# Kernel optimization log

Measured on AMD Instinct MI355X. Metric: run time of the kernel, lower is better.

The kernel has to match this reference:

```python
import jax, jax.numpy as jnp
import numpy as np

NUM_ATOMS = 100000
NUM_BONDS = 200000
MAX_NB = 6
ATOM_FDIM = 133
BOND_FDIM = 147
HIDDEN = 300
DEPTH = 4
NUM_MOLS = 8192


def setup_inputs() -> dict:
    key = jax.random.key(0)
    ks = jax.random.split(key, 10)
    f_atoms = jax.random.normal(ks[0], (NUM_ATOMS, ATOM_FDIM), dtype=jnp.float32)
    f_bonds = jax.random.normal(ks[1], (NUM_BONDS, BOND_FDIM), dtype=jnp.float32)
    a2b = jax.random.randint(ks[2], (NUM_ATOMS, MAX_NB), 0, NUM_BONDS, dtype=jnp.int32)
    b2a = jax.random.randint(ks[3], (NUM_BONDS,), 0, NUM_ATOMS, dtype=jnp.int32)
    b2revb = jax.random.randint(ks[4], (NUM_BONDS,), 0, NUM_BONDS, dtype=jnp.int32)
    mol_ids = jnp.sort(jax.random.randint(ks[5], (NUM_ATOMS,), 0, NUM_MOLS, dtype=jnp.int32))
    s = 1.0 / np.sqrt(HIDDEN)
    W_i = jax.random.uniform(ks[6], (BOND_FDIM, HIDDEN), jnp.float32, -s, s)
    W_h = jax.random.uniform(ks[7], (HIDDEN, HIDDEN), jnp.float32, -s, s)
    W_o = jax.random.uniform(ks[8], (ATOM_FDIM + HIDDEN, HIDDEN), jnp.float32, -s, s)
    b_o = jax.random.uniform(ks[9], (HIDDEN,), jnp.float32, -s, s)
    return {"f_atoms": f_atoms, "f_bonds": f_bonds, "W_i": W_i, "W_h": W_h,
            "W_o": W_o, "b_o": b_o, "a2b": a2b, "b2a": b2a, "b2revb": b2revb,
            "mol_ids": mol_ids}


def reference(f_atoms, f_bonds, W_i, W_h, W_o, b_o, a2b, b2a, b2revb, mol_ids):
    # initial bond messages: W_i then activation (bias=False)
    inp = f_bonds @ W_i                       # [B, H]
    message = jax.nn.relu(inp)
    for _ in range(DEPTH - 1):
        nei = message[a2b]                    # [A, MAX_NB, H] gather
        a_message = nei.sum(axis=1)           # [A, H]
        rev_message = message[b2revb]         # [B, H]
        message = a_message[b2a] - rev_message
        message = jax.nn.relu(inp + message @ W_h)
    # final atom readout
    a_message = message[a2b].sum(axis=1)      # [A, H]
    a_input = jnp.concatenate([f_atoms, a_message], axis=1)
    atom_hiddens = jax.nn.relu(a_input @ W_o + b_o)
    # per-molecule mean aggregation (== chemprop a_scope loop with 'mean')
    sums = jax.ops.segment_sum(atom_hiddens, mol_ids, num_segments=NUM_MOLS)
    counts = jax.ops.segment_sum(jnp.ones((NUM_ATOMS,), jnp.float32), mol_ids,
                                 num_segments=NUM_MOLS)
    return sums / jnp.maximum(counts, 1.0)[:, None]
```

## Files before the change

### kernel.cpp

```cpp
#include <hip/hip_runtime.h>


#define DEVFN static __device__ __forceinline__

typedef __attribute__((ext_vector_type(8))) __bf16 bf16x8;
typedef __attribute__((ext_vector_type(4))) float floatx4;

DEVFN unsigned short f2bf(float f) {
    unsigned int u = __float_as_uint(f);
    u += 0x7FFFu + ((u >> 16) & 1u);
    return (unsigned short)(u >> 16);
}
DEVFN float bf2f(unsigned int u) { return __uint_as_float(u << 16); }

DEVFN unsigned int bfsub2(unsigned int a, unsigned int m) {
    float lo = bf2f(a & 0xffffu) - bf2f(m & 0xffffu);
    float hi = bf2f(a >> 16) - bf2f(m >> 16);
    return (unsigned int)f2bf(lo) | ((unsigned int)f2bf(hi) << 16);
}
DEVFN uint4 bfsub8(uint4 a, uint4 m) {
    return make_uint4(bfsub2(a.x, m.x), bfsub2(a.y, m.y),
                      bfsub2(a.z, m.z), bfsub2(a.w, m.w));
}

__global__ __launch_bounds__(256) void dbg_fill(float* out, int n, float v) {
    int t = blockIdx.x * 256 + threadIdx.x;
    if (t < n) out[t] = v;
}

__global__ __launch_bounds__(256) void prep_wih(const float* __restrict__ Wi,
                                                const float* __restrict__ Wh,
                                                unsigned short* __restrict__ Wt) {
    int t = blockIdx.x * 256 + threadIdx.x;
    if (t >= 320 * 480) return;
    int n = t / 480, k = t - n * 480;
    float v = 0.f;
    if (n < 300) {
        if (k < 147) v = Wi[k * 300 + n];
        else if (k >= 160 && k < 460) v = Wh[(k - 160) * 300 + n];
    }
    Wt[t] = f2bf(v);
}

__global__ __launch_bounds__(256) void prep_wto(const float* __restrict__ Wo,
                                                unsigned short* __restrict__ Wt) {
    int t = blockIdx.x * 256 + threadIdx.x;
    if (t >= 320 * 448) return;
    int n = t / 448, k = t - n * 448;
    float v = 0.f;
    if (n < 300) {
        if (k < 300) v = Wo[(133 + k) * 300 + n];
        else if (k >= 304 && k < 437) v = Wo[(k - 304) * 300 + n];
    }
    Wt[t] = f2bf(v);
}

__global__ __launch_bounds__(256) void pad_bonds(const float* __restrict__ fb,
                                                 unsigned short* __restrict__ out) {
    int t = blockIdx.x * 256 + threadIdx.x;
    if (t >= 200000 * 20) return;
    int b = t / 20, c = t - b * 20;
    unsigned int o[4];
#pragma unroll
    for (int p = 0; p < 4; ++p) {
        int sc = c * 8 + p * 2;
        float v0 = (sc < 147) ? fb[(size_t)b * 147 + sc] : 0.f;
        float v1 = (sc + 1 < 147) ? fb[(size_t)b * 147 + sc + 1] : 0.f;
        o[p] = (unsigned int)f2bf(v0) | ((unsigned int)f2bf(v1) << 16);
    }
    *(uint4*)(out + (size_t)b * 160 + c * 8) = make_uint4(o[0], o[1], o[2], o[3]);
}

__global__ __launch_bounds__(256) void atoms_concat(const float* __restrict__ fa,
                                                    unsigned short* __restrict__ concat) {
    int t = blockIdx.x * 256 + threadIdx.x;
    if (t >= 100000 * 18) return;
    int a = t / 18, c = t - a * 18;
    unsigned int o[4];
#pragma unroll
    for (int p = 0; p < 4; ++p) {
        int sc = c * 8 + p * 2;
        float v0 = (sc < 133) ? fa[(size_t)a * 133 + sc] : 0.f;
        float v1 = (sc + 1 < 133) ? fa[(size_t)a * 133 + sc + 1] : 0.f;
        o[p] = (unsigned int)f2bf(v0) | ((unsigned int)f2bf(v1) << 16);
    }
    *(uint4*)(concat + (size_t)a * 448 + 304 + c * 8) = make_uint4(o[0], o[1], o[2], o[3]);
}

template <int CH>
__global__ __launch_bounds__(256) void gather_sum(const unsigned short* __restrict__ msg,
                                                  const int* __restrict__ a2b,
                                                  unsigned short* __restrict__ out,
                                                  int ostride, int nA) {
    int t = blockIdx.x * 256 + threadIdx.x;
    if (t >= nA * CH) return;
    int a = t / CH, c = t - a * CH;
    float s[8] = {0, 0, 0, 0, 0, 0, 0, 0};
#pragma unroll
    for (int j = 0; j < 6; ++j) {
        int b = a2b[a * 6 + j];
        uint4 v = *(const uint4*)(msg + (size_t)b * 320 + c * 8);
        s[0] += bf2f(v.x & 0xffffu); s[1] += bf2f(v.x >> 16);
        s[2] += bf2f(v.y & 0xffffu); s[3] += bf2f(v.y >> 16);
        s[4] += bf2f(v.z & 0xffffu); s[5] += bf2f(v.z >> 16);
        s[6] += bf2f(v.w & 0xffffu); s[7] += bf2f(v.w >> 16);
    }
    unsigned int o[4];
#pragma unroll
    for (int p = 0; p < 4; ++p)
        o[p] = (unsigned int)f2bf(s[2 * p]) | ((unsigned int)f2bf(s[2 * p + 1]) << 16);
    *(uint4*)(out + (size_t)a * ostride + c * 8) = make_uint4(o[0], o[1], o[2], o[3]);
}

template <int KT0, int KT1, int MODE, int BSTRIDE>
__global__ __launch_bounds__(256) void gemm_k(const unsigned short* __restrict__ A0,
                                              int a0s,
                                              const unsigned short* __restrict__ amsg,
                                              const unsigned short* __restrict__ msg,
                                              const int* __restrict__ b2a,
                                              const int* __restrict__ b2revb,
                                              const unsigned short* __restrict__ Wt,
                                              unsigned short* __restrict__ outp,
                                              float* __restrict__ hid,
                                              const float* __restrict__ bo, int M) {
    constexpr int KT = KT0 + KT1;
    __shared__ unsigned short As[2 * 5120];
    __shared__ unsigned short Bs[2 * 5120];

    const int tid = threadIdx.x;
    const int lane = tid & 63;
    const int wave = tid >> 6;
    const int wm = wave & 1, wn = wave >> 1;
    const int l16 = lane & 15, quad = lane >> 4;
    const int m0 = blockIdx.x * 128;
    const int n0 = blockIdx.y * 160;

    const int arow = tid >> 1, ahalf = tid & 1;
    const int gr = min(m0 + arow, M - 1);
    const unsigned short* a0p = A0 + (size_t)gr * a0s + ahalf * 16;
    const unsigned short* a1p = nullptr;
    const unsigned short* m1p = nullptr;
    if (KT1 > 0) {
        a1p = amsg + (size_t)b2a[gr] * 320 + ahalf * 16;
        m1p = msg + (size_t)b2revb[gr] * 320 + ahalf * 16;
    }
    const int u0 = tid, u1 = tid + 256, u2 = tid + 512;
    const unsigned short* bg0 = Wt + (size_t)(n0 + (u0 >> 2)) * BSTRIDE + ((u0 ^ (u0 >> 2)) & 3) * 8;
    const unsigned short* bg1 = Wt + (size_t)(n0 + (u1 >> 2)) * BSTRIDE + ((u1 ^ (u1 >> 2)) & 3) * 8;
    const unsigned short* bg2 = (tid < 128)
        ? Wt + (size_t)(n0 + (u2 >> 2)) * BSTRIDE + ((u2 ^ (u2 >> 2)) & 3) * 8 : Wt;

    int aoff[4], boff[5];
#pragma unroll
    for (int tm = 0; tm < 4; ++tm)
        aoff[tm] = (wm * 64 + tm * 16 + l16) * 40 + quad * 8;
#pragma unroll
    for (int tn = 0; tn < 5; ++tn) {
        int nl = wn * 80 + tn * 16 + l16;
        boff[tn] = nl * 32 + ((quad ^ nl) & 3) * 8;
    }

    floatx4 acc[4][5];
#pragma unroll
    for (int tm = 0; tm < 4; ++tm)
#pragma unroll
        for (int tn = 0; tn < 5; ++tn) acc[tm][tn] = (floatx4){0.f, 0.f, 0.f, 0.f};

    uint4 ar0, ar1, br0, br1, br2;
    auto ldG = [&](int kt) {
        if (kt < KT0) {
            ar0 = *(const uint4*)(a0p + kt * 32);
            ar1 = *(const uint4*)(a0p + kt * 32 + 8);
        } else {
            int ko = (kt - KT0) * 32;
            uint4 va0 = *(const uint4*)(a1p + ko);
            uint4 va1 = *(const uint4*)(a1p + ko + 8);
            uint4 vm0 = *(const uint4*)(m1p + ko);
            uint4 vm1 = *(const uint4*)(m1p + ko + 8);
            ar0 = bfsub8(va0, vm0);
            ar1 = bfsub8(va1, vm1);
        }
        br0 = *(const uint4*)(bg0 + kt * 32);
        br1 = *(const uint4*)(bg1 + kt * 32);
        if (tid < 128) br2 = *(const uint4*)(bg2 + kt * 32);
    };
    auto stW = [&](int buf) {
        unsigned short* ab = As + buf * 5120 + arow * 40 + ahalf * 16;
        *(uint4*)(ab) = ar0;
        *(uint4*)(ab + 8) = ar1;
        unsigned short* bb = Bs + buf * 5120;
        *(uint4*)(bb + u0 * 8) = br0;
        *(uint4*)(bb + u1 * 8) = br1;
        if (tid < 128) *(uint4*)(bb + u2 * 8) = br2;
    };

    ldG(0);
    stW(0);
    __syncthreads();

#pragma unroll
    for (int kt = 0; kt < KT; ++kt) {
        const int buf = kt & 1;
        if (kt + 1 < KT) ldG(kt + 1);

        bf16x8 av[4], bv[5];
#pragma unroll
        for (int tm = 0; tm < 4; ++tm)
            av[tm] = *(const bf16x8*)(As + buf * 5120 + aoff[tm]);
#pragma unroll
        for (int tn = 0; tn < 5; ++tn)
            bv[tn] = *(const bf16x8*)(Bs + buf * 5120 + boff[tn]);
#pragma unroll
        for (int tn = 0; tn < 5; ++tn)
#pragma unroll
            for (int tm = 0; tm < 4; ++tm)
                acc[tm][tn] = __builtin_amdgcn_mfma_f32_16x16x32_bf16(av[tm], bv[tn], acc[tm][tn], 0, 0, 0);

        if (kt + 1 < KT) stW(buf ^ 1);
        __syncthreads();
    }

    float bias[5];
    if (MODE == 2) {
#pragma unroll
        for (int tn = 0; tn < 5; ++tn) {
            int col = n0 + wn * 80 + tn * 16 + l16;
            bias[tn] = (col < 300) ? bo[col] : 0.f;
        }
    }
#pragma unroll
    for (int tm = 0; tm < 4; ++tm) {
        const int r0 = m0 + wm * 64 + tm * 16 + quad * 4;
#pragma unroll
        for (int tn = 0; tn < 5; ++tn) {
            const int col = n0 + wn * 80 + tn * 16 + l16;
#pragma unroll
            for (int i = 0; i < 4; ++i) {
                int r = r0 + i;
                if (r >= M) continue;
                float c = acc[tm][tn][i];
                if (MODE == 2) {
                    if (col < 300) hid[(size_t)r * 300 + col] = fmaxf(c + bias[tn], 0.f);
                } else {
                    outp[(size_t)r * 320 + col] = f2bf(fmaxf(c, 0.f));
                }
            }
        }
    }
}

__global__ __launch_bounds__(320) void mean_k(const float* __restrict__ hid,
                                              const int* __restrict__ mol_ids,
                                              float* __restrict__ out, int nA) {
    int mol = blockIdx.x;
    int lo, hi;
    {
        int l = 0, h = nA;
        while (l < h) { int m = (l + h) >> 1; if (mol_ids[m] < mol) l = m + 1; else h = m; }
        lo = l;
    }
    {
        int l = lo, h = nA;
        while (l < h) { int m = (l + h) >> 1; if (mol_ids[m] < mol + 1) l = m + 1; else h = m; }
        hi = l;
    }
    int col = threadIdx.x;
    if (col >= 300) return;
    float s = 0.f;
    for (int a = lo; a < hi; ++a) s += hid[(size_t)a * 300 + col];
    int cnt = hi - lo;
    out[(size_t)mol * 300 + col] = s / (float)(cnt > 0 ? cnt : 1);
}

extern "C" void kernel_launch(void* const* d_in, const int* in_sizes, int n_in,
                              void* d_out, int out_size, void* d_ws, size_t ws_size,
                              hipStream_t stream) {
    (void)in_sizes; (void)n_in;
    const float* f_atoms = (const float*)d_in[0];
    const float* f_bonds = (const float*)d_in[1];
    const float* W_i     = (const float*)d_in[2];
    const float* W_h     = (const float*)d_in[3];
    const float* W_o     = (const float*)d_in[4];
    const float* b_o     = (const float*)d_in[5];
    const int*   a2b     = (const int*)d_in[6];
    const int*   b2a     = (const int*)d_in[7];
    const int*   b2revb  = (const int*)d_in[8];
    const int*   mol_ids = (const int*)d_in[9];

    const size_t sz_wih  = 320ull * 480 * 2;
    const size_t sz_wto  = 320ull * 448 * 2;
    const size_t sz_fbp  = 200000ull * 160 * 2;
    const size_t sz_amsg = 100000ull * 320 * 2;
    const size_t sz_msg  = 200000ull * 320 * 2;
    const size_t need = sz_wih + sz_wto + sz_fbp + sz_amsg + 2 * sz_msg;

    if (ws_size < need) {
        dbg_fill<<<(out_size + 255) / 256, 256, 0, stream>>>(
            (float*)d_out, out_size, (float)(ws_size >> 20));
        return;
    }

    char* ws = (char*)d_ws;
    unsigned short* wih  = (unsigned short*)(ws);
    unsigned short* wto  = (unsigned short*)(ws + sz_wih);
    unsigned short* fbp  = (unsigned short*)(ws + sz_wih + sz_wto);
    unsigned short* amsg = (unsigned short*)(ws + sz_wih + sz_wto + sz_fbp);
    unsigned short* msgA = (unsigned short*)(ws + sz_wih + sz_wto + sz_fbp + sz_amsg);
    unsigned short* msgB = (unsigned short*)(ws + sz_wih + sz_wto + sz_fbp + sz_amsg + sz_msg);
    unsigned short* concat = msgA;
    float*          hid    = (float*)msgB;

    prep_wih<<<600, 256, 0, stream>>>(W_i, W_h, wih);
    prep_wto<<<560, 256, 0, stream>>>(W_o, wto);
    pad_bonds<<<15625, 256, 0, stream>>>(f_bonds, fbp);

    gemm_k<5, 0, 0, 480><<<dim3(1563, 2), 256, 0, stream>>>(
        fbp, 160, nullptr, nullptr, nullptr, nullptr, wih, msgA, nullptr, nullptr, 200000);

    unsigned short* cur = msgA;
    unsigned short* other = msgB;
    for (int d = 0; d < 3; ++d) {
        gather_sum<40><<<15625, 256, 0, stream>>>(cur, a2b, amsg, 320, 100000);
        gemm_k<5, 10, 0, 480><<<dim3(1563, 2), 256, 0, stream>>>(
            fbp, 160, amsg, cur, b2a, b2revb, wih, other, nullptr, nullptr, 200000);
        unsigned short* t = cur; cur = other; other = t;
    }

    gather_sum<38><<<14844, 256, 0, stream>>>(cur, a2b, concat, 448, 100000);
    atoms_concat<<<7032, 256, 0, stream>>>(f_atoms, concat);
    gemm_k<14, 0, 2, 448><<<dim3(782, 2), 256, 0, stream>>>(
        concat, 448, nullptr, nullptr, nullptr, nullptr, wto, nullptr, hid, b_o, 100000);
    mean_k<<<8192, 320, 0, stream>>>(hid, mol_ids, (float*)d_out, 100000);
}
```

Baseline: 1.237 ms.

## Stage GEMM tiles via direct global-to-LDS loads and split out gather-subtract

The GEMM kernel now loads A and B tiles with global_load_lds builtins straight into swizzled LDS buffers, instead of staging them through registers. Because the fused gather-and-subtract for the message update cannot be done on a direct load, it moves into a separate combine kernel that writes a materialized message buffer. Launch bounds now request higher occupancy, and workspace buffers are reassigned. The trade is an extra full bond-message write and read per depth step in exchange for a simpler, lower-register GEMM load path.

```diff
diff --git a/kernel.cpp b/kernel.cpp
--- a/kernel.cpp
+++ b/kernel.cpp
@@ -18,9 +18,11 @@
     float hi = bf2f(a >> 16) - bf2f(m >> 16);
     return (unsigned int)f2bf(lo) | ((unsigned int)f2bf(hi) << 16);
 }
-DEVFN uint4 bfsub8(uint4 a, uint4 m) {
-    return make_uint4(bfsub2(a.x, m.x), bfsub2(a.y, m.y),
-                      bfsub2(a.z, m.z), bfsub2(a.w, m.w));
+
+DEVFN void gll(const unsigned short* g, void* l) {
+    __builtin_amdgcn_global_load_lds(
+        (const __attribute__((address_space(1))) unsigned int*)g,
+        (__attribute__((address_space(3))) unsigned int*)l, 16, 0, 0);
 }
 
 __global__ __launch_bounds__(256) void dbg_fill(float* out, int n, float v) {
@@ -112,53 +114,82 @@
     *(uint4*)(out + (size_t)a * ostride + c * 8) = make_uint4(o[0], o[1], o[2], o[3]);
 }
 
+__global__ __launch_bounds__(256) void combine(const unsigned short* __restrict__ amsg,
+                                               const unsigned short* __restrict__ msg,
+                                               const int* __restrict__ b2a,
+                                               const int* __restrict__ b2revb,
+                                               unsigned short* __restrict__ out) {
+    int t = blockIdx.x * 256 + threadIdx.x;
+    if (t >= 200000 * 40) return;
+    int b = t / 40, c = t - b * 40;
+    int sa = b2a[b], rb = b2revb[b];
+    uint4 va = *(const uint4*)(amsg + (size_t)sa * 320 + c * 8);
+    uint4 vm = *(const uint4*)(msg + (size_t)rb * 320 + c * 8);
+    uint4 o = make_uint4(bfsub2(va.x, vm.x), bfsub2(va.y, vm.y),
+                         bfsub2(va.z, vm.z), bfsub2(va.w, vm.w));
+    *(uint4*)(out + (size_t)b * 320 + c * 8) = o;
+}
+
 template <int KT0, int KT1, int MODE, int BSTRIDE>
-__global__ __launch_bounds__(256) void gemm_k(const unsigned short* __restrict__ A0,
-                                              int a0s,
-                                              const unsigned short* __restrict__ amsg,
-                                              const unsigned short* __restrict__ msg,
-                                              const int* __restrict__ b2a,
-                                              const int* __restrict__ b2revb,
-                                              const unsigned short* __restrict__ Wt,
-                                              unsigned short* __restrict__ outp,
-                                              float* __restrict__ hid,
-                                              const float* __restrict__ bo, int M) {
+__global__ __launch_bounds__(256, 4) void gemm_k(const unsigned short* __restrict__ A0,
+                                                 int a0s,
+                                                 const unsigned short* __restrict__ A1,
+                                                 int a1s,
+                                                 const unsigned short* __restrict__ Wt,
+                                                 unsigned short* __restrict__ outp,
+                                                 float* __restrict__ hid,
+                                                 const float* __restrict__ bo, int M) {
     constexpr int KT = KT0 + KT1;
-    __shared__ unsigned short As[2 * 5120];
-    __shared__ unsigned short Bs[2 * 5120];
+    __shared__ char lds[2 * 8192 + 2 * 10240];
+    char* As = lds;
+    char* Bs = lds + 16384;
 
     const int tid = threadIdx.x;
     const int lane = tid & 63;
-    const int wave = tid >> 6;
-    const int wm = wave & 1, wn = wave >> 1;
+    const int w = tid >> 6;
+    const int wm = w & 1, wn = w >> 1;
     const int l16 = lane & 15, quad = lane >> 4;
     const int m0 = blockIdx.x * 128;
     const int n0 = blockIdx.y * 160;
 
-    const int arow = tid >> 1, ahalf = tid & 1;
-    const int gr = min(m0 + arow, M - 1);
-    const unsigned short* a0p = A0 + (size_t)gr * a0s + ahalf * 16;
-    const unsigned short* a1p = nullptr;
-    const unsigned short* m1p = nullptr;
-    if (KT1 > 0) {
-        a1p = amsg + (size_t)b2a[gr] * 320 + ahalf * 16;
-        m1p = msg + (size_t)b2revb[gr] * 320 + ahalf * 16;
-    }
-    const int u0 = tid, u1 = tid + 256, u2 = tid + 512;
-    const unsigned short* bg0 = Wt + (size_t)(n0 + (u0 >> 2)) * BSTRIDE + ((u0 ^ (u0 >> 2)) & 3) * 8;
-    const unsigned short* bg1 = Wt + (size_t)(n0 + (u1 >> 2)) * BSTRIDE + ((u1 ^ (u1 >> 2)) & 3) * 8;
-    const unsigned short* bg2 = (tid < 128)
-        ? Wt + (size_t)(n0 + (u2 >> 2)) * BSTRIDE + ((u2 ^ (u2 >> 2)) & 3) * 8 : Wt;
-
+    const int qg = ((tid & 3) ^ (tid >> 2) ^ (tid >> 4)) & 3;
+    const int r0i = tid >> 2;
+    const int gr0 = min(m0 + r0i, M - 1);
+    const int gr1 = min(m0 + 64 + r0i, M - 1);
+    const unsigned short* pA0a = A0 + (size_t)gr0 * a0s + qg * 8;
+    const unsigned short* pA0b = A0 + (size_t)gr1 * a0s + qg * 8;
+    const unsigned short* pA1a = (KT1 > 0) ? A1 + (size_t)gr0 * a1s + qg * 8 : A0;
+    const unsigned short* pA1b = (KT1 > 0) ? A1 + (size_t)gr1 * a1s + qg * 8 : A0;
+    const unsigned short* pB0 = Wt + (size_t)(n0 + r0i) * BSTRIDE + qg * 8;
+    const unsigned short* pB1 = Wt + (size_t)(n0 + 64 + r0i) * BSTRIDE + qg * 8;
+    const unsigned short* pB2 = (tid < 128)
+        ? Wt + (size_t)(n0 + 128 + r0i) * BSTRIDE + qg * 8 : Wt;
+
+    const int wl = w * 1024;
+
+    auto issue = [&](int kt, int buf) {
+        char* ab = As + buf * 8192;
+        char* bb = Bs + buf * 10240;
+        if (kt < KT0) {
+            gll(pA0a + kt * 32, ab + wl);
+            gll(pA0b + kt * 32, ab + 4096 + wl);
+        } else {
+            gll(pA1a + (kt - KT0) * 32, ab + wl);
+            gll(pA1b + (kt - KT0) * 32, ab + 4096 + wl);
+        }
+        gll(pB0 + kt * 32, bb + wl);
+        gll(pB1 + kt * 32, bb + 4096 + wl);
+        if (tid < 128) gll(pB2 + kt * 32, bb + 8192 + wl);
+    };
+
+    const int swz = ((quad ^ l16 ^ (l16 >> 2)) & 3) * 16;
     int aoff[4], boff[5];
 #pragma unroll
     for (int tm = 0; tm < 4; ++tm)
-        aoff[tm] = (wm * 64 + tm * 16 + l16) * 40 + quad * 8;
-#pragma unroll
-    for (int tn = 0; tn < 5; ++tn) {
-        int nl = wn * 80 + tn * 16 + l16;
-        boff[tn] = nl * 32 + ((quad ^ nl) & 3) * 8;
-    }
+        aoff[tm] = (wm * 64 + tm * 16 + l16) * 64 + swz;
+#pragma unroll
+    for (int tn = 0; tn < 5; ++tn)
+        boff[tn] = (wn * 80 + tn * 16 + l16) * 64 + swz;
 
     floatx4 acc[4][5];
 #pragma unroll
@@ -166,57 +197,27 @@
 #pragma unroll
         for (int tn = 0; tn < 5; ++tn) acc[tm][tn] = (floatx4){0.f, 0.f, 0.f, 0.f};
 
-    uint4 ar0, ar1, br0, br1, br2;
-    auto ldG = [&](int kt) {
-        if (kt < KT0) {
-            ar0 = *(const uint4*)(a0p + kt * 32);
-            ar1 = *(const uint4*)(a0p + kt * 32 + 8);
-        } else {
-            int ko = (kt - KT0) * 32;
-            uint4 va0 = *(const uint4*)(a1p + ko);
-            uint4 va1 = *(const uint4*)(a1p + ko + 8);
-            uint4 vm0 = *(const uint4*)(m1p + ko);
-            uint4 vm1 = *(const uint4*)(m1p + ko + 8);
-            ar0 = bfsub8(va0, vm0);
-            ar1 = bfsub8(va1, vm1);
-        }
-        br0 = *(const uint4*)(bg0 + kt * 32);
-        br1 = *(const uint4*)(bg1 + kt * 32);
-        if (tid < 128) br2 = *(const uint4*)(bg2 + kt * 32);
-    };
-    auto stW = [&](int buf) {
-        unsigned short* ab = As + buf * 5120 + arow * 40 + ahalf * 16;
-        *(uint4*)(ab) = ar0;
-        *(uint4*)(ab + 8) = ar1;
-        unsigned short* bb = Bs + buf * 5120;
-        *(uint4*)(bb + u0 * 8) = br0;
-        *(uint4*)(bb + u1 * 8) = br1;
-        if (tid < 128) *(uint4*)(bb + u2 * 8) = br2;
-    };
-
-    ldG(0);
-    stW(0);
+    issue(0, 0);
     __syncthreads();
 
 #pragma unroll
     for (int kt = 0; kt < KT; ++kt) {
         const int buf = kt & 1;
-        if (kt + 1 < KT) ldG(kt + 1);
-
-        bf16x8 av[4], bv[5];
+        if (kt + 1 < KT) issue(kt + 1, buf ^ 1);
+
+        const char* ap = As + buf * 8192;
+        const char* bp = Bs + buf * 10240;
+        bf16x8 av[4];
 #pragma unroll
         for (int tm = 0; tm < 4; ++tm)
-            av[tm] = *(const bf16x8*)(As + buf * 5120 + aoff[tm]);
-#pragma unroll
-        for (int tn = 0; tn < 5; ++tn)
-            bv[tn] = *(const bf16x8*)(Bs + buf * 5120 + boff[tn]);
-#pragma unroll
-        for (int tn = 0; tn < 5; ++tn)
+            av[tm] = *(const bf16x8*)(ap + aoff[tm]);
+#pragma unroll
+        for (int tn = 0; tn < 5; ++tn) {
+            bf16x8 bv = *(const bf16x8*)(bp + boff[tn]);
 #pragma unroll
             for (int tm = 0; tm < 4; ++tm)
-                acc[tm][tn] = __builtin_amdgcn_mfma_f32_16x16x32_bf16(av[tm], bv[tn], acc[tm][tn], 0, 0, 0);
-
-        if (kt + 1 < KT) stW(buf ^ 1);
+                acc[tm][tn] = __builtin_amdgcn_mfma_f32_16x16x32_bf16(av[tm], bv, acc[tm][tn], 0, 0, 0);
+        }
         __syncthreads();
     }
 
@@ -307,28 +308,26 @@
     unsigned short* amsg = (unsigned short*)(ws + sz_wih + sz_wto + sz_fbp);
     unsigned short* msgA = (unsigned short*)(ws + sz_wih + sz_wto + sz_fbp + sz_amsg);
     unsigned short* msgB = (unsigned short*)(ws + sz_wih + sz_wto + sz_fbp + sz_amsg + sz_msg);
-    unsigned short* concat = msgA;
-    float*          hid    = (float*)msgB;
+    unsigned short* concat = msgB;
+    float*          hid    = (float*)fbp;
 
     prep_wih<<<600, 256, 0, stream>>>(W_i, W_h, wih);
     prep_wto<<<560, 256, 0, stream>>>(W_o, wto);
     pad_bonds<<<15625, 256, 0, stream>>>(f_bonds, fbp);
 
     gemm_k<5, 0, 0, 480><<<dim3(1563, 2), 256, 0, stream>>>(
-        fbp, 160, nullptr, nullptr, nullptr, nullptr, wih, msgA, nullptr, nullptr, 200000);
-
-    unsigned short* cur = msgA;
-    unsigned short* other = msgB;
+        fbp, 160, nullptr, 0, wih, msgA, nullptr, nullptr, 200000);
+
     for (int d = 0; d < 3; ++d) {
-        gather_sum<40><<<15625, 256, 0, stream>>>(cur, a2b, amsg, 320, 100000);
+        gather_sum<40><<<15625, 256, 0, stream>>>(msgA, a2b, amsg, 320, 100000);
+        combine<<<31250, 256, 0, stream>>>(amsg, msgA, b2a, b2revb, msgB);
         gemm_k<5, 10, 0, 480><<<dim3(1563, 2), 256, 0, stream>>>(
-            fbp, 160, amsg, cur, b2a, b2revb, wih, other, nullptr, nullptr, 200000);
-        unsigned short* t = cur; cur = other; other = t;
-    }
-
-    gather_sum<38><<<14844, 256, 0, stream>>>(cur, a2b, concat, 448, 100000);
+            fbp, 160, msgB, 320, wih, msgA, nullptr, nullptr, 200000);
+    }
+
+    gather_sum<38><<<14844, 256, 0, stream>>>(msgA, a2b, concat, 448, 100000);
     atoms_concat<<<7032, 256, 0, stream>>>(f_atoms, concat);
     gemm_k<14, 0, 2, 448><<<dim3(782, 2), 256, 0, stream>>>(
-        concat, 448, nullptr, nullptr, nullptr, nullptr, wto, nullptr, hid, b_o, 100000);
+        concat, 448, nullptr, 0, wto, nullptr, hid, b_o, 100000);
     mean_k<<<8192, 320, 0, stream>>>(hid, mol_ids, (float*)d_out, 100000);
 }
```

Result: slower. 1.567 ms (+26.7%).
